# Optimization experiments

Measured on AMD Instinct MI355X. Metric: run time of the kernel, lower is better.

The kernel has to match this reference:

```python
import jax, jax.numpy as jnp
import numpy as np
import math

B, S, D, H, DFF, L = 8, 1024, 512, 8, 2048, 4
DK = D // H
EPS = 1e-5
NEG = -1e32


def _sinusoidal_pe(s, d):
    pos = np.arange(s)[:, None].astype(np.float32)
    div = np.exp(np.arange(0, d, 2).astype(np.float32) * (-math.log(10000.0) / d))
    pe = np.zeros((s, d), np.float32)
    pe[:, 0::2] = np.sin(pos * div)
    pe[:, 1::2] = np.cos(pos * div)
    return jnp.asarray(pe)


def setup_inputs() -> dict:
    key = jax.random.key(0)
    ks = jax.random.split(key, 20)
    sd = 0.02
    inp = {
        "q_embed_data": jax.random.normal(ks[0], (B, S, D), jnp.float32),
        "qa_embed_data": jax.random.normal(ks[1], (B, S, D), jnp.float32),
        "pe": _sinusoidal_pe(S, D),
        # stacked per-layer params (leading dim L). kq_same=1 -> q uses Wk.
        "Wk": sd * jax.random.normal(ks[2], (L, D, D), jnp.float32),
        "bk": jnp.zeros((L, D), jnp.float32),
        "Wv": sd * jax.random.normal(ks[3], (L, D, D), jnp.float32),
        "bv": jnp.zeros((L, D), jnp.float32),
        "Wo": sd * jax.random.normal(ks[4], (L, D, D), jnp.float32),
        "bo": jnp.zeros((L, D), jnp.float32),
        "ln1_s": jnp.ones((L, D), jnp.float32),
        "ln1_b": jnp.zeros((L, D), jnp.float32),
        "W1": sd * jax.random.normal(ks[5], (L, D, DFF), jnp.float32),
        "b1": jnp.zeros((L, DFF), jnp.float32),
        "W2": sd * jax.random.normal(ks[6], (L, DFF, D), jnp.float32),
        "b2": jnp.zeros((L, D), jnp.float32),
        "ln2_s": jnp.ones((L, D), jnp.float32),
        "ln2_b": jnp.zeros((L, D), jnp.float32),
    }
    return inp


def _layernorm(z, s, b):
    m = z.mean(-1, keepdims=True)
    v = ((z - m) ** 2).mean(-1, keepdims=True)
    return (z - m) / jnp.sqrt(v + EPS) * s + b


def _forward(q_embed_data, qa_embed_data, pe, Wk, bk, Wv, bv, Wo, bo,
             ln1_s, ln1_b, W1, b1, W2, b2, ln2_s, ln2_b):
    x = q_embed_data + pe[None, :, :]
    y = qa_embed_data + pe[None, :, :]  # values source stays fixed across blocks
    allowed = jnp.tril(jnp.ones((S, S), bool), -1)  # strictly-causal: attend only to j < i
    row_keep = (jnp.arange(S) > 0).astype(x.dtype)[None, None, :, None]  # zero_pad row 0

    def heads(z, W, b):
        return (z @ W + b).reshape(B, S, H, DK).transpose(0, 2, 1, 3)  # [B,H,S,DK]

    def step(xc, p):
        wk, bk_, wv, bv_, wo, bo_, s1, b1n, w1, b1f, w2, b2f, s2, b2n = p
        q = heads(xc, wk, bk_)  # kq_same: q via k_linear
        k = heads(xc, wk, bk_)
        v = heads(y, wv, bv_)
        sc = jnp.einsum('bhid,bhjd->bhij', q, k) / math.sqrt(DK)
        att = jax.nn.softmax(jnp.where(allowed, sc, NEG), axis=-1) * row_keep
        o = jnp.einsum('bhij,bhjd->bhid', att, v).transpose(0, 2, 1, 3).reshape(B, S, D)
        x1 = _layernorm(xc + (o @ wo + bo_), s1, b1n)
        f = jax.nn.relu(x1 @ w1 + b1f) @ w2 + b2f
        x2 = _layernorm(x1 + f, s2, b2n)
        return x2, None

    out, _ = jax.lax.scan(step, x, (Wk, bk, Wv, bv, Wo, bo, ln1_s, ln1_b, W1, b1, W2, b2, ln2_s, ln2_b))
    return out


def reference(q_embed_data, qa_embed_data, pe, Wk, bk, Wv, bv, Wo, bo,
              ln1_s, ln1_b, W1, b1, W2, b2, ln2_s, ln2_b):
    return _forward(q_embed_data, qa_embed_data, pe, Wk, bk, Wv, bv, Wo, bo,
                    ln1_s, ln1_b, W1, b1, W2, b2, ln2_s, ln2_b)
```

## Files before the change

kernel.cpp:

```cpp
#include <hip/hip_runtime.h>
#include <stdint.h>

typedef __attribute__((ext_vector_type(8))) __bf16 bf16x8;
typedef __attribute__((ext_vector_type(4))) float f32x4;
typedef __attribute__((ext_vector_type(4))) unsigned int u32x4;

constexpr int B = 8, S = 1024, D = 512, H = 8, DFF = 2048, L = 4, DK = 64;
constexpr int MR = B * S;
constexpr int NSLOT = 80;

__device__ __forceinline__ unsigned short f2bf(float f) {
    union { float f; unsigned u; } v; v.f = f;
    unsigned u = v.u;
    u += 0x7fffu + ((u >> 16) & 1u);
    return (unsigned short)(u >> 16);
}

__device__ __forceinline__ void gload_lds16(const void* g, void* l) {
    __builtin_amdgcn_global_load_lds(
        (const __attribute__((address_space(1))) void*)g,
        (__attribute__((address_space(3))) void*)l, 16, 0, 0);
}

__global__ __launch_bounds__(256) void add_pe_kernel(
    const float* __restrict__ qe, const float* __restrict__ qa,
    const float* __restrict__ pe, float* __restrict__ x_f32,
    unsigned short* __restrict__ x_bf, unsigned short* __restrict__ y_bf) {
    int gid = blockIdx.x * 256 + threadIdx.x;
    int base = gid * 4;
    int po = base & (S * D - 1);
    float4 p = *(const float4*)(pe + po);
    float4 a = *(const float4*)(qe + base);
    float4 q = *(const float4*)(qa + base);
    float4 xv = make_float4(a.x + p.x, a.y + p.y, a.z + p.z, a.w + p.w);
    float4 yv = make_float4(q.x + p.x, q.y + p.y, q.z + p.z, q.w + p.w);
    *(float4*)(x_f32 + base) = xv;
    ushort4 xb; xb.x = f2bf(xv.x); xb.y = f2bf(xv.y); xb.z = f2bf(xv.z); xb.w = f2bf(xv.w);
    ushort4 yb; yb.x = f2bf(yv.x); yb.y = f2bf(yv.y); yb.z = f2bf(yv.z); yb.w = f2bf(yv.w);
    *(ushort4*)(x_bf + base) = xb;
    *(ushort4*)(y_bf + base) = yb;
}

__global__ __launch_bounds__(256) void wtrans_kernel(
    const float* __restrict__ src, unsigned short* __restrict__ dst, int K, int N) {
    __shared__ float t[64][65];
    src += (size_t)blockIdx.z * K * N;
    dst += (size_t)blockIdx.z * K * N;
    int n0 = blockIdx.x * 64, k0 = blockIdx.y * 64;
    int tid = threadIdx.x;
    int r = tid >> 4, c4 = (tid & 15) * 4;
    #pragma unroll
    for (int rr = 0; rr < 64; rr += 16) {
        float4 v = *(const float4*)(src + (size_t)(k0 + r + rr) * N + n0 + c4);
        t[r + rr][c4] = v.x; t[r + rr][c4 + 1] = v.y;
        t[r + rr][c4 + 2] = v.z; t[r + rr][c4 + 3] = v.w;
    }
    __syncthreads();
    int n = tid >> 2, kc = (tid & 3) * 16;
    ushort4 o[4];
    #pragma unroll
    for (int g = 0; g < 4; g++) {
        o[g].x = f2bf(t[kc + g * 4 + 0][n]);
        o[g].y = f2bf(t[kc + g * 4 + 1][n]);
        o[g].z = f2bf(t[kc + g * 4 + 2][n]);
        o[g].w = f2bf(t[kc + g * 4 + 3][n]);
    }
    unsigned short* dp = dst + (size_t)(n0 + n) * K + k0 + kc;
    #pragma unroll
    for (int g = 0; g < 4; g++) *(ushort4*)(dp + g * 4) = o[g];
}

template<int BN, bool RELU, bool RESID, bool OUT_F32, bool OUT_BF16, bool OUT_VT>
__global__ __launch_bounds__(256) void gemm_kernel(
    const unsigned short* __restrict__ A, const unsigned short* __restrict__ Bt,
    const float* __restrict__ bias, const float* __restrict__ resid,
    float* __restrict__ out_f32, unsigned short* __restrict__ out_bf,
    int M, int N, int K) {
    constexpr int MT = (BN == 128) ? 4 : 2;
    constexpr int WROWS = (BN == 128) ? 64 : 32;
    constexpr int BRND = (BN == 128) ? 4 : 2;
    __shared__ unsigned short a_lds[128 * 64];
    __shared__ unsigned short b_lds[BN * 64];

    const int tid = threadIdx.x;
    const int lane = tid & 63, wid = tid >> 6;
    const int wm = (BN == 128) ? (wid >> 1) : wid;
    const int wn = (BN == 128) ? (wid & 1) : 0;
    const int l15 = lane & 15, quad = lane >> 4;
    const int nmt = gridDim.x, nnt = gridDim.y;
    const int o_lin = blockIdx.y * nmt + blockIdx.x;
    const int xcd = o_lin & 7, oi = o_lin >> 3;
    const int mtile = xcd * (nmt >> 3) + oi / nnt;
    const int ntile = oi % nnt;
    const int m0 = mtile * 128, n0 = ntile * BN;

    f32x4 acc[MT][4];
    #pragma unroll
    for (int i = 0; i < MT; i++)
        #pragma unroll
        for (int j = 0; j < 4; j++) { f32x4 z = {0.f, 0.f, 0.f, 0.f}; acc[i][j] = z; }

    const unsigned short* aP[4];
    unsigned short* aL[4];
    #pragma unroll
    for (int j = 0; j < 4; j++) {
        int c = wid * 256 + j * 64 + lane;
        int r = c >> 3, slot = c & 7, kg = slot ^ (r & 7);
        aP[j] = A + (size_t)(m0 + r) * K + kg * 8;
        aL[j] = a_lds + (size_t)(wid * 256 + j * 64) * 8;
    }
    const unsigned short* bP[BRND];
    unsigned short* bL[BRND];
    #pragma unroll
    for (int j = 0; j < BRND; j++) {
        int c = wid * (BRND * 64) + j * 64 + lane;
        int r = c >> 3, slot = c & 7, kg = slot ^ (r & 7);
        bP[j] = Bt + (size_t)(n0 + r) * K + kg * 8;
        bL[j] = b_lds + (size_t)(wid * (BRND * 64) + j * 64) * 8;
    }

    for (int k0 = 0; k0 < K; k0 += 64) {
        #pragma unroll
        for (int j = 0; j < 4; j++) gload_lds16(aP[j] + k0, aL[j]);
        #pragma unroll
        for (int j = 0; j < BRND; j++) gload_lds16(bP[j] + k0, bL[j]);
        __syncthreads();

        bf16x8 af[MT][2], bfv[4][2];
        #pragma unroll
        for (int mt = 0; mt < MT; mt++) {
            int row = wm * WROWS + mt * 16 + l15;
            #pragma unroll
            for (int kh = 0; kh < 2; kh++)
                af[mt][kh] = *(const bf16x8*)&a_lds[row * 64 + (((kh * 4 + quad) ^ (row & 7)) * 8)];
        }
        #pragma unroll
        for (int nt = 0; nt < 4; nt++) {
            int row = wn * 64 + nt * 16 + l15;
            #pragma unroll
            for (int kh = 0; kh < 2; kh++)
                bfv[nt][kh] = *(const bf16x8*)&b_lds[row * 64 + (((kh * 4 + quad) ^ (row & 7)) * 8)];
        }
        #pragma unroll
        for (int mt = 0; mt < MT; mt++)
            #pragma unroll
            for (int nt = 0; nt < 4; nt++) {
                acc[mt][nt] = __builtin_amdgcn_mfma_f32_16x16x32_bf16(af[mt][0], bfv[nt][0], acc[mt][nt], 0, 0, 0);
                acc[mt][nt] = __builtin_amdgcn_mfma_f32_16x16x32_bf16(af[mt][1], bfv[nt][1], acc[mt][nt], 0, 0, 0);
            }
        __syncthreads();
    }

    #pragma unroll
    for (int nt = 0; nt < 4; nt++) {
        int col = n0 + wn * 64 + nt * 16 + l15;
        float bv = bias[col];
        #pragma unroll
        for (int mt = 0; mt < MT; mt++) {
            int row0 = m0 + wm * WROWS + mt * 16 + quad * 4;
            if (OUT_VT) {
                int hh = col >> 6, d = col & 63;
                int bb = row0 >> 10, s0 = row0 & 1023;
                ushort4 o;
                o.x = f2bf(acc[mt][nt][0] + bv);
                o.y = f2bf(acc[mt][nt][1] + bv);
                o.z = f2bf(acc[mt][nt][2] + bv);
                o.w = f2bf(acc[mt][nt][3] + bv);
                *(ushort4*)(out_bf + ((size_t)(bb * H + hh) * DK + d) * S + s0) = o;
            } else {
                #pragma unroll
                for (int r = 0; r < 4; r++) {
                    int row = row0 + r;
                    float v = acc[mt][nt][r] + bv;
                    if (RESID) v += resid[(size_t)row * N + col];
                    if (RELU) v = fmaxf(v, 0.f);
                    size_t o = (size_t)row * N + col;
                    if (OUT_F32) out_f32[o] = v;
                    if (OUT_BF16) out_bf[o] = f2bf(v);
                }
            }
        }
    }
}

__global__ __launch_bounds__(256) void ln_kernel(
    const float* __restrict__ in, const float* __restrict__ gamma,
    const float* __restrict__ beta, float* __restrict__ out_f32,
    unsigned short* __restrict__ out_bf) {
    __shared__ float red[8];
    int row = blockIdx.x, tid = threadIdx.x;
    const float* p = in + (size_t)row * D;
    float2 v = *(const float2*)(p + tid * 2);
    float s = v.x + v.y;
    float q = v.x * v.x + v.y * v.y;
    #pragma unroll
    for (int off = 32; off > 0; off >>= 1) {
        s += __shfl_xor(s, off);
        q += __shfl_xor(q, off);
    }
    int wid = tid >> 6, lane = tid & 63;
    if (lane == 0) { red[wid] = s; red[4 + wid] = q; }
    __syncthreads();
    s = red[0] + red[1] + red[2] + red[3];
    q = red[4] + red[5] + red[6] + red[7];
    float mean = s * (1.f / D);
    float var = q * (1.f / D) - mean * mean;
    float inv = rsqrtf(var + 1e-5f);
    int c = tid * 2;
    float2 g = *(const float2*)(gamma + c);
    float2 bb = *(const float2*)(beta + c);
    float o0 = (v.x - mean) * inv * g.x + bb.x;
    float o1 = (v.y - mean) * inv * g.y + bb.y;
    *(float2*)(out_f32 + (size_t)row * D + c) = make_float2(o0, o1);
    ushort2 ob; ob.x = f2bf(o0); ob.y = f2bf(o1);
    *(ushort2*)(out_bf + (size_t)row * D + c) = ob;
}

__device__ __forceinline__ void load_kfrag(const unsigned short* kbase, int kt,
                                           int l15, int quad, bf16x8 (&kf)[4][2]) {
    #pragma unroll
    for (int mt = 0; mt < 4; mt++) {
        const unsigned short* kr = kbase + (size_t)(kt * 64 + mt * 16 + l15) * D;
        kf[mt][0] = *(const bf16x8*)(kr + quad * 8);
        kf[mt][1] = *(const bf16x8*)(kr + 32 + quad * 8);
    }
}
__device__ __forceinline__ void load_vfrag(const unsigned short* vbase, int kt,
                                           int l15, int quad, bf16x8 (&vf)[4][2]) {
    #pragma unroll
    for (int mt = 0; mt < 4; mt++) {
        const unsigned short* vr = vbase + (size_t)(mt * 16 + l15) * S + kt * 64;
        vf[mt][0] = *(const bf16x8*)(vr + quad * 8);
        vf[mt][1] = *(const bf16x8*)(vr + 32 + quad * 8);
    }
}

__global__ __launch_bounds__(64, 2) void attn_part_kernel(
    const unsigned short* __restrict__ qk, const unsigned short* __restrict__ vt,
    float* __restrict__ part_o, float* __restrict__ part_l) {
    __shared__ unsigned p_u32[2][32 * 36];
    constexpr float C = 0.18033688011112042f;
    const float NEGINF = -__builtin_huge_valf();

    int bx = blockIdx.x;
    int s = (NSLOT - 1) - (bx >> 6);
    int hh = bx & 63;
    int b = hh >> 3, h = hh & 7;
    int head = hh;
    int lane = threadIdx.x;
    int l15 = lane & 15, quad = lane >> 4;

    int t, c, nc;
    if (s < 8)       { t = s;                c = 0;           nc = 1; }
    else if (s < 24) { t = 8 + ((s - 8) >> 1);  c = (s - 8) & 1;   nc = 2; }
    else if (s < 48) { t = 16 + (s - 24) / 3;   c = (s - 24) % 3;  nc = 3; }
    else             { t = 24 + ((s - 48) >> 2); c = (s - 48) & 3; nc = 4; }
    const int nt = (t >> 1) + 1;
    const int ck0 = (c * nt) / nc, ck1 = ((c + 1) * nt) / nc;

    const int rowbase = b * S, colbase = h * DK;
    const unsigned short* kbase = qk + (size_t)rowbase * D + colbase;
    const unsigned short* vbase = vt + (size_t)head * (DK * S);

    bf16x8 qf[2][2];
    #pragma unroll
    for (int u = 0; u < 2; u++) {
        const unsigned short* qrow =
            qk + (size_t)(rowbase + t * 32 + u * 16 + l15) * D + colbase;
        qf[u][0] = *(const bf16x8*)(qrow + quad * 8);
        qf[u][1] = *(const bf16x8*)(qrow + 32 + quad * 8);
    }

    float l_r[2] = {0.f, 0.f};
    f32x4 o_acc[2][4];
    #pragma unroll
    for (int u = 0; u < 2; u++)
        #pragma unroll
        for (int i = 0; i < 4; i++) { f32x4 z = {0.f, 0.f, 0.f, 0.f}; o_acc[u][i] = z; }

    auto process = [&](int kt, bf16x8 (&kf)[4][2], bf16x8 (&vf)[4][2], int par) {
        const bool diag = 2 * kt + 2 > t;
        unsigned* pb = p_u32[par];
        #pragma unroll
        for (int u = 0; u < 2; u++) {
            const int qb = t * 32 + u * 16;
            const int ql = u * 16 + l15;
            #pragma unroll
            for (int mt = 0; mt < 4; mt++) {
                if (!diag || (kt * 64 + mt * 16 < qb + 16)) {
                    f32x4 a = {0.f, 0.f, 0.f, 0.f};
                    a = __builtin_amdgcn_mfma_f32_16x16x32_bf16(kf[mt][0], qf[u][0], a, 0, 0, 0);
                    a = __builtin_amdgcn_mfma_f32_16x16x32_bf16(kf[mt][1], qf[u][1], a, 0, 0, 0);
                    if (diag) {
                        const int gi = qb + l15;
                        #pragma unroll
                        for (int r = 0; r < 4; r++) {
                            int gj = kt * 64 + mt * 16 + quad * 4 + r;
                            a[r] = (gj >= gi) ? NEGINF : a[r];
                        }
                    }
                    float e0 = exp2f(a[0] * C), e1 = exp2f(a[1] * C);
                    float e2 = exp2f(a[2] * C), e3 = exp2f(a[3] * C);
                    unsigned pk0, pk1;
                    asm("v_cvt_pk_bf16_f32 %0, %1, %2" : "=v"(pk0) : "v"(e0), "v"(e1));
                    asm("v_cvt_pk_bf16_f32 %0, %1, %2" : "=v"(pk1) : "v"(e2), "v"(e3));
                    l_r[u] += (e0 + e1) + (e2 + e3);
                    *(uint2*)&pb[ql * 36 + mt * 8 + quad * 2] = make_uint2(pk0, pk1);
                } else {
                    *(uint2*)&pb[ql * 36 + mt * 8 + quad * 2] = make_uint2(0u, 0u);
                }
            }
        }
        #pragma unroll
        for (int u = 0; u < 2; u++) {
            const int qb = t * 32 + u * 16;
            const int ql = u * 16 + l15;
            u32x4 d0 = *(const u32x4*)&pb[ql * 36 + quad * 4];
            bf16x8 pb0 = __builtin_bit_cast(bf16x8, d0);
            const bool hi = (kt * 64 + 32 < qb + 16);
            if (hi) {
                u32x4 d1 = *(const u32x4*)&pb[ql * 36 + 16 + quad * 4];
                bf16x8 pb1 = __builtin_bit_cast(bf16x8, d1);
                #pragma unroll
                for (int mt = 0; mt < 4; mt++) {
                    o_acc[u][mt] = __builtin_amdgcn_mfma_f32_16x16x32_bf16(vf[mt][0], pb0, o_acc[u][mt], 0, 0, 0);
                    o_acc[u][mt] = __builtin_amdgcn_mfma_f32_16x16x32_bf16(vf[mt][1], pb1, o_acc[u][mt], 0, 0, 0);
                }
            } else {
                #pragma unroll
                for (int mt = 0; mt < 4; mt++)
                    o_acc[u][mt] = __builtin_amdgcn_mfma_f32_16x16x32_bf16(vf[mt][0], pb0, o_acc[u][mt], 0, 0, 0);
            }
        }
    };

    bf16x8 ka[4][2], kb[4][2], va[4][2];
    load_kfrag(kbase, ck0, l15, quad, ka);
    int kt = ck0;
    while (true) {
        load_vfrag(vbase, kt, l15, quad, va);
        if (kt + 1 < ck1) load_kfrag(kbase, kt + 1, l15, quad, kb);
        process(kt, ka, va, 0);
        if (++kt >= ck1) break;
        load_vfrag(vbase, kt, l15, quad, va);
        if (kt + 1 < ck1) load_kfrag(kbase, kt + 1, l15, quad, ka);
        process(kt, kb, va, 1);
        if (++kt >= ck1) break;
    }

    #pragma unroll
    for (int u = 0; u < 2; u++) {
        l_r[u] += __shfl_xor(l_r[u], 16);
        l_r[u] += __shfl_xor(l_r[u], 32);
    }

    int p = head * NSLOT + s;
    if (quad == 0) {
        #pragma unroll
        for (int u = 0; u < 2; u++)
            part_l[(size_t)p * 32 + u * 16 + l15] = l_r[u];
    }
    float* po = part_o + (size_t)p * 2048;
    #pragma unroll
    for (int u = 0; u < 2; u++)
        #pragma unroll
        for (int mt = 0; mt < 4; mt++)
            #pragma unroll
            for (int r = 0; r < 4; r++)
                po[(mt * 16 + quad * 4 + r) * 32 + u * 16 + l15] = o_acc[u][mt][r];
}

__global__ __launch_bounds__(256) void attn_combine_kernel(
    const float* __restrict__ part_o, const float* __restrict__ part_l,
    unsigned short* __restrict__ ob) {
    int bx = blockIdx.x;
    int t = bx & 31, head = bx >> 5;
    int b = head >> 3, h = head & 7;
    int tid = threadIdx.x;
    int q = tid >> 3, dg = (tid & 7) * 8;
    int g = t >> 3, nc = g + 1;
    int p0 = head * NSLOT + ((g * (g + 1)) << 2) + (t - (g << 3)) * nc;

    float ldenom = 0.f;
    for (int c = 0; c < nc; c++)
        ldenom += part_l[(size_t)(p0 + c) * 32 + q];
    float inv = (ldenom > 0.f) ? 1.f / ldenom : 0.f;
    int si = t * 32 + q;
    if (si == 0) inv = 0.f;

    float v[8] = {0.f, 0.f, 0.f, 0.f, 0.f, 0.f, 0.f, 0.f};
    for (int c = 0; c < nc; c++) {
        const float* po = part_o + (size_t)(p0 + c) * 2048;
        #pragma unroll
        for (int i = 0; i < 8; i++)
            v[i] += po[(dg + i) * 32 + q];
    }
    unsigned short out[8];
    #pragma unroll
    for (int i = 0; i < 8; i++) out[i] = f2bf(v[i] * inv);
    unsigned short* dst = ob + (size_t)(b * S + si) * D + h * DK + dg;
    *(u32x4*)dst = *(const u32x4*)out;
}

extern "C" void kernel_launch(void* const* d_in, const int* in_sizes, int n_in,
                              void* d_out, int out_size, void* d_ws, size_t ws_size,
                              hipStream_t stream) {
    (void)in_sizes; (void)n_in; (void)out_size; (void)ws_size;
    const float* qe  = (const float*)d_in[0];
    const float* qa  = (const float*)d_in[1];
    const float* pe  = (const float*)d_in[2];
    const float* Wk  = (const float*)d_in[3];
    const float* bk  = (const float*)d_in[4];
    const float* Wv  = (const float*)d_in[5];
    const float* bv  = (const float*)d_in[6];
    const float* Wo  = (const float*)d_in[7];
    const float* bo  = (const float*)d_in[8];
    const float* l1s = (const float*)d_in[9];
    const float* l1b = (const float*)d_in[10];
    const float* W1  = (const float*)d_in[11];
    const float* b1  = (const float*)d_in[12];
    const float* W2  = (const float*)d_in[13];
    const float* b2  = (const float*)d_in[14];
    const float* l2s = (const float*)d_in[15];
    const float* l2b = (const float*)d_in[16];

    char* w = (char*)d_ws;
    float* x_f32  = (float*)w;           w += (size_t)MR * D * 4;
    float* t_f32  = (float*)w;           w += (size_t)MR * D * 4;
    float* x1_f32 = (float*)w;           w += (size_t)MR * D * 4;
    unsigned short* x_bf  = (unsigned short*)w; w += (size_t)MR * D * 2;
    unsigned short* y_bf  = (unsigned short*)w; w += (size_t)MR * D * 2;
    unsigned short* qk_bf = (unsigned short*)w; w += (size_t)MR * D * 2;
    unsigned short* vt_bf = (unsigned short*)w; w += (size_t)MR * D * 2;
    unsigned short* o_bf  = (unsigned short*)w; w += (size_t)MR * D * 2;
    unsigned short* x1_bf = (unsigned short*)w; w += (size_t)MR * D * 2;
    char* scratch = w;                          w += (size_t)NSLOT * 64 * 2048 * 4;
    unsigned short* h_bf = (unsigned short*)scratch;
    float* part_o = (float*)scratch;
    unsigned short* wkT = (unsigned short*)w;   w += (size_t)L * D * D * 2;
    unsigned short* wvT = (unsigned short*)w;   w += (size_t)L * D * D * 2;
    unsigned short* woT = (unsigned short*)w;   w += (size_t)L * D * D * 2;
    unsigned short* w1T = (unsigned short*)w;   w += (size_t)L * D * DFF * 2;
    unsigned short* w2T = (unsigned short*)w;   w += (size_t)L * DFF * D * 2;
    float* part_l = (float*)w;                  w += (size_t)NSLOT * 64 * 32 * 4;

    add_pe_kernel<<<MR * D / 4 / 256, 256, 0, stream>>>(qe, qa, pe, x_f32, x_bf, y_bf);
    wtrans_kernel<<<dim3(8, 8, L), 256, 0, stream>>>(Wk, wkT, D, D);
    wtrans_kernel<<<dim3(8, 8, L), 256, 0, stream>>>(Wv, wvT, D, D);
    wtrans_kernel<<<dim3(8, 8, L), 256, 0, stream>>>(Wo, woT, D, D);
    wtrans_kernel<<<dim3(32, 8, L), 256, 0, stream>>>(W1, w1T, D, DFF);
    wtrans_kernel<<<dim3(8, 32, L), 256, 0, stream>>>(W2, w2T, DFF, D);

    dim3 g512(64, 8), g2048(64, 16);
    for (int l = 0; l < L; l++) {
        gemm_kernel<64, false, false, false, true, false><<<g512, 256, 0, stream>>>(
            x_bf, wkT + (size_t)l * D * D, bk + l * D, nullptr, nullptr, qk_bf, MR, D, D);
        gemm_kernel<64, false, false, false, false, true><<<g512, 256, 0, stream>>>(
            y_bf, wvT + (size_t)l * D * D, bv + l * D, nullptr, nullptr, vt_bf, MR, D, D);
        attn_part_kernel<<<NSLOT * 64, 64, 0, stream>>>(qk_bf, vt_bf, part_o, part_l);
        attn_combine_kernel<<<64 * 32, 256, 0, stream>>>(part_o, part_l, o_bf);
        gemm_kernel<64, false, true, true, false, false><<<g512, 256, 0, stream>>>(
            o_bf, woT + (size_t)l * D * D, bo + l * D, x_f32, t_f32, nullptr, MR, D, D);
        ln_kernel<<<MR, 256, 0, stream>>>(t_f32, l1s + l * D, l1b + l * D, x1_f32, x1_bf);
        gemm_kernel<128, true, false, false, true, false><<<g2048, 256, 0, stream>>>(
            x1_bf, w1T + (size_t)l * D * DFF, b1 + l * DFF, nullptr, nullptr, h_bf, MR, DFF, D);
        gemm_kernel<64, false, true, true, false, false><<<g512, 256, 0, stream>>>(
            h_bf, w2T + (size_t)l * DFF * D, b2 + l * D, x1_f32, t_f32, nullptr, MR, D, DFF);
        float* xo = (l == L - 1) ? (float*)d_out : x_f32;
        ln_kernel<<<MR, 256, 0, stream>>>(t_f32, l2s + l * D, l2b + l * D, xo, x_bf);
    }
}
```

Baseline: 853.6 us.

## Share K/V tiles across four waves via double-buffered LDS in attention

```diff
diff --git a/kernel.cpp b/kernel.cpp
--- a/kernel.cpp
+++ b/kernel.cpp
@@ -216,47 +216,37 @@
     *(ushort2*)(out_bf + (size_t)row * D + c) = ob;
 }
 
-__device__ __forceinline__ void load_kfrag(const unsigned short* kbase, int kt,
-                                           int l15, int quad, bf16x8 (&kf)[4][2]) {
-    #pragma unroll
-    for (int mt = 0; mt < 4; mt++) {
-        const unsigned short* kr = kbase + (size_t)(kt * 64 + mt * 16 + l15) * D;
-        kf[mt][0] = *(const bf16x8*)(kr + quad * 8);
-        kf[mt][1] = *(const bf16x8*)(kr + 32 + quad * 8);
-    }
-}
-__device__ __forceinline__ void load_vfrag(const unsigned short* vbase, int kt,
-                                           int l15, int quad, bf16x8 (&vf)[4][2]) {
-    #pragma unroll
-    for (int mt = 0; mt < 4; mt++) {
-        const unsigned short* vr = vbase + (size_t)(mt * 16 + l15) * S + kt * 64;
-        vf[mt][0] = *(const bf16x8*)(vr + quad * 8);
-        vf[mt][1] = *(const bf16x8*)(vr + 32 + quad * 8);
-    }
-}
-
-__global__ __launch_bounds__(64, 2) void attn_part_kernel(
+__global__ __launch_bounds__(256, 2) void attn_part_kernel(
     const unsigned short* __restrict__ qk, const unsigned short* __restrict__ vt,
     float* __restrict__ part_o, float* __restrict__ part_l) {
-    __shared__ unsigned p_u32[2][32 * 36];
+    __shared__ unsigned short kbuf[2][64 * 64];
+    __shared__ unsigned short vbuf[2][64 * 64];
+    __shared__ unsigned p_u32[4][32 * 36];
     constexpr float C = 0.18033688011112042f;
     const float NEGINF = -__builtin_huge_valf();
 
-    int bx = blockIdx.x;
-    int s = (NSLOT - 1) - (bx >> 6);
-    int hh = bx & 63;
-    int b = hh >> 3, h = hh & 7;
-    int head = hh;
-    int lane = threadIdx.x;
-    int l15 = lane & 15, quad = lane >> 4;
-
-    int t, c, nc;
-    if (s < 8)       { t = s;                c = 0;           nc = 1; }
-    else if (s < 24) { t = 8 + ((s - 8) >> 1);  c = (s - 8) & 1;   nc = 2; }
-    else if (s < 48) { t = 16 + (s - 24) / 3;   c = (s - 24) % 3;  nc = 3; }
-    else             { t = 24 + ((s - 48) >> 2); c = (s - 48) & 3; nc = 4; }
-    const int nt = (t >> 1) + 1;
-    const int ck0 = (c * nt) / nc, ck1 = ((c + 1) * nt) / nc;
+    const int bx = blockIdx.x;
+    const int e = 19 - (bx >> 6);
+    const int hh = bx & 63;
+    const int b = hh >> 3, h = hh & 7;
+    const int head = hh;
+    const int tid = threadIdx.x;
+    const int w = tid >> 6, lane = tid & 63;
+    const int l15 = lane & 15, quad = lane >> 4;
+
+    int Qb, st;
+    if (e >= 16)     { Qb = 7; st = 16; }
+    else if (e >= 12){ Qb = 6; st = 12; }
+    else if (e >= 9) { Qb = 5; st = 9;  }
+    else if (e >= 6) { Qb = 4; st = 6;  }
+    else if (e >= 4) { Qb = 3; st = 4;  }
+    else if (e >= 2) { Qb = 2; st = 2;  }
+    else             { Qb = e; st = e;  }
+    const int c = e - st;
+    const int nc = (Qb >> 1) + 1;
+    const int nkt = (Qb + 1) * 2;
+    const int ck0 = (c * nkt) / nc, ck1 = ((c + 1) * nkt) / nc;
+    const int qrow0 = Qb * 128 + w * 32;
 
     const int rowbase = b * S, colbase = h * DK;
     const unsigned short* kbase = qk + (size_t)rowbase * D + colbase;
@@ -266,11 +256,30 @@
     #pragma unroll
     for (int u = 0; u < 2; u++) {
         const unsigned short* qrow =
-            qk + (size_t)(rowbase + t * 32 + u * 16 + l15) * D + colbase;
+            qk + (size_t)(rowbase + qrow0 + u * 16 + l15) * D + colbase;
         qf[u][0] = *(const bf16x8*)(qrow + quad * 8);
         qf[u][1] = *(const bf16x8*)(qrow + 32 + quad * 8);
     }
 
+    const int sr = lane >> 3;
+    const int sseg = (lane & 7) ^ sr;
+    const unsigned short* kgp[2]; const unsigned short* vgp[2];
+    unsigned short* kld[2]; unsigned short* vld[2];
+    #pragma unroll
+    for (int j = 0; j < 2; j++) {
+        int rt = w * 16 + j * 8 + sr;
+        kgp[j] = kbase + (size_t)rt * D + sseg * 8;
+        vgp[j] = vbase + (size_t)rt * S + sseg * 8;
+        kld[j] = &kbuf[0][(w * 16 + j * 8) * 64];
+        vld[j] = &vbuf[0][(w * 16 + j * 8) * 64];
+    }
+    auto stage = [&](int buf, int kt) {
+        #pragma unroll
+        for (int j = 0; j < 2; j++) gload_lds16(kgp[j] + (size_t)kt * 64 * D, kld[j] + buf * 4096);
+        #pragma unroll
+        for (int j = 0; j < 2; j++) gload_lds16(vgp[j] + kt * 64, vld[j] + buf * 4096);
+    };
+
     float l_r[2] = {0.f, 0.f};
     f32x4 o_acc[2][4];
     #pragma unroll
@@ -278,16 +287,24 @@
         #pragma unroll
         for (int i = 0; i < 4; i++) { f32x4 z = {0.f, 0.f, 0.f, 0.f}; o_acc[u][i] = z; }
 
-    auto process = [&](int kt, bf16x8 (&kf)[4][2], bf16x8 (&vf)[4][2], int par) {
-        const bool diag = 2 * kt + 2 > t;
-        unsigned* pb = p_u32[par];
+    auto consume = [&](int kt, const unsigned short* kl, const unsigned short* vl) {
+        unsigned* pb = p_u32[w];
+        bf16x8 kf[4][2];
+        #pragma unroll
+        for (int mt = 0; mt < 4; mt++) {
+            const unsigned short* kr = kl + (mt * 16 + l15) * 64;
+            #pragma unroll
+            for (int kh = 0; kh < 2; kh++)
+                kf[mt][kh] = *(const bf16x8*)(kr + (((kh * 4 + quad) ^ (l15 & 7)) * 8));
+        }
+        const bool diag = kt * 64 + 64 > qrow0;
         #pragma unroll
         for (int u = 0; u < 2; u++) {
-            const int qb = t * 32 + u * 16;
+            const int qb = qrow0 + u * 16;
             const int ql = u * 16 + l15;
             #pragma unroll
             for (int mt = 0; mt < 4; mt++) {
-                if (!diag || (kt * 64 + mt * 16 < qb + 16)) {
+                if (kt * 64 + mt * 16 < qb + 16) {
                     f32x4 a = {0.f, 0.f, 0.f, 0.f};
                     a = __builtin_amdgcn_mfma_f32_16x16x32_bf16(kf[mt][0], qf[u][0], a, 0, 0, 0);
                     a = __builtin_amdgcn_mfma_f32_16x16x32_bf16(kf[mt][1], qf[u][1], a, 0, 0, 0);
@@ -311,9 +328,17 @@
                 }
             }
         }
+        bf16x8 vf[4][2];
+        #pragma unroll
+        for (int mt = 0; mt < 4; mt++) {
+            const unsigned short* vr = vl + (mt * 16 + l15) * 64;
+            #pragma unroll
+            for (int kh = 0; kh < 2; kh++)
+                vf[mt][kh] = *(const bf16x8*)(vr + (((kh * 4 + quad) ^ (l15 & 7)) * 8));
+        }
         #pragma unroll
         for (int u = 0; u < 2; u++) {
-            const int qb = t * 32 + u * 16;
+            const int qb = qrow0 + u * 16;
             const int ql = u * 16 + l15;
             u32x4 d0 = *(const u32x4*)&pb[ql * 36 + quad * 4];
             bf16x8 pb0 = __builtin_bit_cast(bf16x8, d0);
@@ -334,18 +359,23 @@
         }
     };
 
-    bf16x8 ka[4][2], kb[4][2], va[4][2];
-    load_kfrag(kbase, ck0, l15, quad, ka);
-    int kt = ck0;
-    while (true) {
-        load_vfrag(vbase, kt, l15, quad, va);
-        if (kt + 1 < ck1) load_kfrag(kbase, kt + 1, l15, quad, kb);
-        process(kt, ka, va, 0);
-        if (++kt >= ck1) break;
-        load_vfrag(vbase, kt, l15, quad, va);
-        if (kt + 1 < ck1) load_kfrag(kbase, kt + 1, l15, quad, ka);
-        process(kt, kb, va, 1);
-        if (++kt >= ck1) break;
+    stage(0, ck0);
+    for (int kt = ck0; kt < ck1; ++kt) {
+        const int cur = (kt - ck0) & 1;
+        if (kt + 1 < ck1) {
+            stage(cur ^ 1, kt + 1);
+            asm volatile("s_waitcnt vmcnt(4)" ::: "memory");
+        } else {
+            asm volatile("s_waitcnt vmcnt(0)" ::: "memory");
+        }
+        __builtin_amdgcn_sched_barrier(0);
+        __builtin_amdgcn_s_barrier();
+        __builtin_amdgcn_sched_barrier(0);
+        if (kt * 64 < qrow0 + 32)
+            consume(kt, &kbuf[cur][0], &vbuf[cur][0]);
+        __builtin_amdgcn_sched_barrier(0);
+        __builtin_amdgcn_s_barrier();
+        __builtin_amdgcn_sched_barrier(0);
     }
 
     #pragma unroll
@@ -354,7 +384,7 @@
         l_r[u] += __shfl_xor(l_r[u], 32);
     }
 
-    int p = head * NSLOT + s;
+    const int p = head * NSLOT + 4 * st + c * 4 + w;
     if (quad == 0) {
         #pragma unroll
         for (int u = 0; u < 2; u++)
@@ -378,19 +408,22 @@
     int b = head >> 3, h = head & 7;
     int tid = threadIdx.x;
     int q = tid >> 3, dg = (tid & 7) * 8;
-    int g = t >> 3, nc = g + 1;
-    int p0 = head * NSLOT + ((g * (g + 1)) << 2) + (t - (g << 3)) * nc;
+    int Qb = t >> 2, w = t & 3;
+    int nc = (Qb >> 1) + 1;
+    int m = Qb >> 1;
+    int st = m * m + ((Qb & 1) ? Qb : m);
+    int p0 = head * NSLOT + 4 * st + w;
 
     float ldenom = 0.f;
     for (int c = 0; c < nc; c++)
-        ldenom += part_l[(size_t)(p0 + c) * 32 + q];
+        ldenom += part_l[(size_t)(p0 + 4 * c) * 32 + q];
     float inv = (ldenom > 0.f) ? 1.f / ldenom : 0.f;
     int si = t * 32 + q;
     if (si == 0) inv = 0.f;
 
     float v[8] = {0.f, 0.f, 0.f, 0.f, 0.f, 0.f, 0.f, 0.f};
     for (int c = 0; c < nc; c++) {
-        const float* po = part_o + (size_t)(p0 + c) * 2048;
+        const float* po = part_o + (size_t)(p0 + 4 * c) * 2048;
         #pragma unroll
         for (int i = 0; i < 8; i++)
             v[i] += po[(dg + i) * 32 + q];
@@ -457,7 +490,7 @@
             x_bf, wkT + (size_t)l * D * D, bk + l * D, nullptr, nullptr, qk_bf, MR, D, D);
         gemm_kernel<64, false, false, false, false, true><<<g512, 256, 0, stream>>>(
             y_bf, wvT + (size_t)l * D * D, bv + l * D, nullptr, nullptr, vt_bf, MR, D, D);
-        attn_part_kernel<<<NSLOT * 64, 64, 0, stream>>>(qk_bf, vt_bf, part_o, part_l);
+        attn_part_kernel<<<20 * 64, 256, 0, stream>>>(qk_bf, vt_bf, part_o, part_l);
         attn_combine_kernel<<<64 * 32, 256, 0, stream>>>(part_o, part_l, o_bf);
         gemm_kernel<64, false, true, true, false, false><<<g512, 256, 0, stream>>>(
             o_bf, woT + (size_t)l * D * D, bo + l * D, x_f32, t_f32, nullptr, MR, D, D);
```

After: 771.2 us. 9.7% less time.
